# Kernel tuning notes

Measured on AMD Instinct MI355X. Metric: run time of the kernel, lower is better.

Reference implementation:

```python
import jax, jax.numpy as jnp
import numpy as np

B, L, D, H = 4, 2048, 1024, 16
DK = D // H  # 64


def setup_inputs() -> dict:
    key = jax.random.key(0)
    ks = jax.random.split(key, 8)
    s = 0.05
    return {
        "query": jax.random.normal(ks[0], (B, L, D), jnp.float32),
        "key": jax.random.normal(ks[1], (B, L, D), jnp.float32),
        "value": jax.random.normal(ks[2], (B, L, D), jnp.float32),
        "mask": jnp.ones((B, L, L), jnp.int32),
        "Wq": jax.random.normal(ks[3], (D, DK), jnp.float32) * s,
        "Wk": jax.random.normal(ks[4], (D, DK), jnp.float32) * s,
        "Wv": jax.random.normal(ks[5], (D, DK), jnp.float32) * s,
        "Wo": jax.random.normal(ks[6], (H * DK, D), jnp.float32) * s,
    }


def reference(query, key, value, mask, Wq, Wk, Wv, Wo):
    # Single-head projections (the torch module projects once, then reuses
    # the SAME q/k/v for every head, producing num_heads identical outputs).
    q = jnp.einsum("bld,dk->blk", query, Wq)   # [B, L, DK]
    k = jnp.einsum("bld,dk->blk", key, Wk)
    v = jnp.einsum("bld,dk->blk", value, Wv)
    scale = 1.0 / jnp.sqrt(jnp.asarray(DK, q.dtype))
    scores = jnp.einsum("bqk,bsk->bqs", q, k) * scale  # [B, L, L]
    scores = jnp.where(mask == 0, -jnp.inf, scores)
    p = jax.nn.softmax(scores, axis=-1)
    head = jnp.einsum("bqs,bsk->bqk", p, v)    # [B, L, DK]
    # Concatenation of H identical heads == tile along last dim.
    out = jnp.tile(head, (1, 1, H))             # [B, L, H*DK]
    return jnp.einsum("blh,hd->bld", out, Wo)
```

## Files before the change

### kernel.cpp

```cpp
#include <hip/hip_runtime.h>
#include <hip/hip_bf16.h>

#define Bb 4
#define Ll 2048
#define Dd 1024
#define DKk 64
#define BL (Bb*Ll)
#define G_SPLIT 8
#define KSPLIT 4

typedef __attribute__((ext_vector_type(4))) float f32x4;
typedef __attribute__((ext_vector_type(8))) short bf16x8;

__device__ __forceinline__ unsigned short f2bf(float x) {
  unsigned int u = __builtin_bit_cast(unsigned int, x);
  u += 0x7fffu + ((u >> 16) & 1u);
  return (unsigned short)(u >> 16);
}
__device__ __forceinline__ unsigned int pack2bf(float a, float b) {
  return (unsigned int)f2bf(a) | ((unsigned int)f2bf(b) << 16);
}

__global__ __launch_bounds__(256)
void prep_kernel(const float* __restrict__ Wq, const float* __restrict__ Wk,
                 const float* __restrict__ Wv, const float* __restrict__ Wo,
                 unsigned short* __restrict__ WqT, unsigned short* __restrict__ WkT,
                 unsigned short* __restrict__ WvT, unsigned short* __restrict__ WoSumT) {
  int idx = blockIdx.x * 256 + threadIdx.x;
  if (idx < 3 * 65536) {
    int which = idx >> 16;
    int r = idx & 65535;
    int n = r & 63, k = r >> 6;
    const float* W = which == 0 ? Wq : (which == 1 ? Wk : Wv);
    unsigned short* WT = which == 0 ? WqT : (which == 1 ? WkT : WvT);
    WT[(size_t)n * 1024 + k] = f2bf(W[(size_t)k * 64 + n]);
  } else {
    int r = idx - 3 * 65536;
    int d = r & 1023, k = r >> 10;
    float s = 0.f;
#pragma unroll
    for (int h = 0; h < 16; ++h) s += Wo[(size_t)(h * 64 + k) * 1024 + d];
    WoSumT[(size_t)d * 64 + k] = f2bf(s);
  }
}

__global__ __launch_bounds__(256)
void maskpack_kernel(const int* __restrict__ mask, unsigned long long* __restrict__ BM) {
  const int wid = (blockIdx.x * 256 + threadIdx.x) >> 6;
  const int lane = threadIdx.x & 63;
  const int nw = (gridDim.x * 256) >> 6;
  for (int task = wid; task < BL * 8; task += nw) {
    const int4 m = *(const int4*)(mask + (size_t)task * 256 + lane * 4);
    unsigned long long b0 = __ballot(m.x != 0);
    unsigned long long b1 = __ballot(m.y != 0);
    unsigned long long b2 = __ballot(m.z != 0);
    unsigned long long b3 = __ballot(m.w != 0);
    unsigned long long v = lane == 0 ? b0 : lane == 1 ? b1 : lane == 2 ? b2 : b3;
    if (lane < 4) BM[(size_t)task * 4 + lane] = v;
  }
}

__global__ __launch_bounds__(256)
void proj_kernel(const float* __restrict__ query, const float* __restrict__ key,
                 const float* __restrict__ value,
                 const unsigned short* __restrict__ WqT, const unsigned short* __restrict__ WkT,
                 const unsigned short* __restrict__ WvT,
                 float* __restrict__ Pp) {
  const int which = blockIdx.y;
  const int ks = blockIdx.z;
  const float* X = which == 0 ? query : (which == 1 ? key : value);
  const unsigned short* WT = which == 0 ? WqT : (which == 1 ? WkT : WvT);
  const int R0 = blockIdx.x * 64;

  __shared__ __align__(16) unsigned short Xl[64 * 72];
  __shared__ __align__(16) unsigned short Wl[64 * 72];

  const int tid = threadIdx.x;
  const int lane = tid & 63;
  const int w = tid >> 6;
  const int g = lane >> 4, lr = lane & 15;

  f32x4 acc[4];
#pragma unroll
  for (int t = 0; t < 4; ++t) acc[t] = (f32x4){0.f, 0.f, 0.f, 0.f};

  for (int it = 0; it < 4; ++it) {
    const int k0 = ks * 256 + it * 64;
    if (it) __syncthreads();
#pragma unroll
    for (int i = 0; i < 4; ++i) {
      int c = tid + 256 * i;
      int row = c >> 4, cc = c & 15;
      f32x4 v = *(const f32x4*)(X + (size_t)(R0 + row) * 1024 + k0 + cc * 4);
      uint2 pv;
      pv.x = pack2bf(v[0], v[1]);
      pv.y = pack2bf(v[2], v[3]);
      *(uint2*)&Xl[row * 72 + cc * 4] = pv;
    }
#pragma unroll
    for (int i = 0; i < 2; ++i) {
      int c = tid + 256 * i;
      int row = c >> 3, cc = c & 7;
      *(uint4*)&Wl[row * 72 + cc * 8] = *(const uint4*)(WT + (size_t)row * 1024 + k0 + cc * 8);
    }
    __syncthreads();
#pragma unroll
    for (int kh = 0; kh < 2; ++kh) {
      bf16x8 a = *(const bf16x8*)&Xl[(w * 16 + lr) * 72 + kh * 32 + g * 8];
#pragma unroll
      for (int t = 0; t < 4; ++t) {
        bf16x8 b = *(const bf16x8*)&Wl[(t * 16 + lr) * 72 + kh * 32 + g * 8];
        acc[t] = __builtin_amdgcn_mfma_f32_16x16x32_bf16(a, b, acc[t], 0, 0, 0);
      }
    }
  }

  float* pb = Pp + ((size_t)(which * KSPLIT + ks) * BL + R0 + w * 16) * 64;
#pragma unroll
  for (int t = 0; t < 4; ++t)
#pragma unroll
    for (int i = 0; i < 4; ++i)
      pb[(g * 4 + i) * 64 + t * 16 + lr] = acc[t][i];
}

__global__ __launch_bounds__(256)
void projcomb_kernel(const float* __restrict__ Pp,
                     unsigned short* __restrict__ Qp, unsigned short* __restrict__ Kf,
                     unsigned short* __restrict__ Vf) {
  const int which = blockIdx.y;
  int idx = blockIdx.x * 256 + threadIdx.x;
  int row = idx >> 4, c0 = (idx & 15) * 4;
  const float* base = Pp + ((size_t)which * KSPLIT * BL + row) * 64 + c0;
  f32x4 s = (f32x4){0.f, 0.f, 0.f, 0.f};
#pragma unroll
  for (int gg = 0; gg < KSPLIT; ++gg) {
    f32x4 a = *(const f32x4*)(base + (size_t)gg * BL * 64);
    s[0] += a[0]; s[1] += a[1]; s[2] += a[2]; s[3] += a[3];
  }
  const int b = row >> 11, sl = row & 2047;
  if (which == 0) {
    uint2 pv;
    pv.x = pack2bf(s[0], s[1]);
    pv.y = pack2bf(s[2], s[3]);
    *(uint2*)(Qp + (size_t)row * 64 + c0) = pv;
  } else if (which == 1) {
    const int c = (sl >> 4) & 3, lr = sl & 15, tile = b * 32 + (sl >> 6);
    const int gg = c0 >> 3, e0 = c0 & 7;
    uint2 pv;
    pv.x = pack2bf(s[0], s[1]);
    pv.y = pack2bf(s[2], s[3]);
    *(uint2*)(Kf + (size_t)tile * 4096 + (c * 8 + gg) * 128 + lr * 8 + e0) = pv;
  } else {
    const int h = (sl >> 5) & 1, g2 = (sl >> 3) & 3, e = sl & 7, tile = b * 32 + (sl >> 6);
#pragma unroll
    for (int j = 0; j < 4; ++j) {
      int dk = c0 + j, t = dk >> 4, lrv = dk & 15;
      Vf[(size_t)tile * 4096 + ((t * 2 + h) * 4 + g2) * 128 + lrv * 8 + e] = f2bf(s[j]);
    }
  }
}

__global__ __launch_bounds__(128, 4)
void attn_kernel(const unsigned short* __restrict__ Qp, const unsigned short* __restrict__ Kf,
                 const unsigned short* __restrict__ Vf, const unsigned long long* __restrict__ BM,
                 float* __restrict__ Opart, float* __restrict__ lpart) {
  const int q0 = blockIdx.x * 32;
  const int gy = blockIdx.y;
  const int b = q0 >> 11;
  const int tid = threadIdx.x, lane = tid & 63, w = tid >> 6;
  const int g = lane >> 4, lr = lane & 15;

  const unsigned short* qrow = Qp + (size_t)(q0 + w * 16 + lr) * 64;
  bf16x8 qf0 = *(const bf16x8*)(qrow + g * 8);
  bf16x8 qf1 = *(const bf16x8*)(qrow + 32 + g * 8);

  const unsigned long long* bm = BM + ((size_t)(q0 + w * 16 + lr) * 8 + gy) * 4;
  const unsigned long long W0 = bm[0], W1 = bm[1], W2 = bm[2], W3 = bm[3];

  f32x4 o[4];
#pragma unroll
  for (int t = 0; t < 4; ++t) o[t] = (f32x4){0.f, 0.f, 0.f, 0.f};
  float lsum = 0.f;

  const unsigned short* Kt = Kf + (size_t)(b * 32 + gy * 4) * 4096;
  const unsigned short* Vt = Vf + (size_t)(b * 32 + gy * 4) * 4096;

#pragma unroll
  for (int st = 0; st < 4; ++st) {
    const unsigned short* Kts = Kt + st * 4096;
    const unsigned short* Vts = Vt + st * 4096;

    bf16x8 kf0[4], kf1[4];
#pragma unroll
    for (int c = 0; c < 4; ++c) {
      kf0[c] = *(const bf16x8*)(Kts + (c * 8 + g) * 128 + lr * 8);
      kf1[c] = *(const bf16x8*)(Kts + (c * 8 + 4 + g) * 128 + lr * 8);
    }

    uint2 packs[4];
#pragma unroll
    for (int c = 0; c < 4; ++c) {
      f32x4 a4 = (f32x4){0.f, 0.f, 0.f, 0.f};
      a4 = __builtin_amdgcn_mfma_f32_16x16x32_bf16(kf0[c], qf0, a4, 0, 0, 0);
      a4 = __builtin_amdgcn_mfma_f32_16x16x32_bf16(kf1[c], qf1, a4, 0, 0, 0);
      const int j = st * 16 + 4 * c + g;
      float p0 = ((W0 >> j) & 1) ? __expf(a4[0] * 0.125f) : 0.f;
      float p1 = ((W1 >> j) & 1) ? __expf(a4[1] * 0.125f) : 0.f;
      float p2 = ((W2 >> j) & 1) ? __expf(a4[2] * 0.125f) : 0.f;
      float p3 = ((W3 >> j) & 1) ? __expf(a4[3] * 0.125f) : 0.f;
      lsum += (p0 + p1) + (p2 + p3);
      packs[c].x = pack2bf(p0, p1);
      packs[c].y = pack2bf(p2, p3);
    }

#pragma unroll
    for (int h = 0; h < 2; ++h) {
      const int srcLo = lr + ((g & 1) << 5);
      const int srcHi = srcLo + 16;
      uint2 pl0 = packs[2 * h], pl1 = packs[2 * h + 1];
      unsigned a0x = __shfl((int)pl0.x, srcLo), a0y = __shfl((int)pl0.y, srcLo);
      unsigned a1x = __shfl((int)pl1.x, srcLo), a1y = __shfl((int)pl1.y, srcLo);
      unsigned b0x = __shfl((int)pl0.x, srcHi), b0y = __shfl((int)pl0.y, srcHi);
      unsigned b1x = __shfl((int)pl1.x, srcHi), b1y = __shfl((int)pl1.y, srcHi);
      const bool hisel = ((g >> 1) & 1) != 0;
      uint4 bb;
      bb.x = hisel ? a1x : a0x;
      bb.y = hisel ? a1y : a0y;
      bb.z = hisel ? b1x : b0x;
      bb.w = hisel ? b1y : b0y;
      bf16x8 pb = __builtin_bit_cast(bf16x8, bb);
#pragma unroll
      for (int t = 0; t < 4; ++t) {
        bf16x8 av = *(const bf16x8*)(Vts + ((t * 2 + h) * 4 + g) * 128 + lr * 8);
        o[t] = __builtin_amdgcn_mfma_f32_16x16x32_bf16(av, pb, o[t], 0, 0, 0);
      }
    }
  }

  lsum += __shfl_xor(lsum, 16);
  lsum += __shfl_xor(lsum, 32);

  float* Ob = Opart + ((size_t)gy * BL + q0 + w * 16 + lr) * 64;
#pragma unroll
  for (int t = 0; t < 4; ++t)
    *(f32x4*)(Ob + t * 16 + g * 4) = o[t];
  if (lane < 16)
    lpart[(size_t)gy * BL + q0 + w * 16 + lane] = lsum;
}

__global__ __launch_bounds__(256)
void combine_kernel(const float* __restrict__ Opart, const float* __restrict__ lpart,
                    unsigned short* __restrict__ Hp) {
  int idx = blockIdx.x * 256 + threadIdx.x;
  int q = idx >> 4, c0 = (idx & 15) * 4;
  float l = 0.f;
#pragma unroll
  for (int gg = 0; gg < G_SPLIT; ++gg) l += lpart[(size_t)gg * BL + q];
  float inv = 1.f / l;
  f32x4 s = (f32x4){0.f, 0.f, 0.f, 0.f};
#pragma unroll
  for (int gg = 0; gg < G_SPLIT; ++gg) {
    f32x4 a = *(const f32x4*)(Opart + ((size_t)gg * BL + q) * 64 + c0);
    s[0] += a[0]; s[1] += a[1]; s[2] += a[2]; s[3] += a[3];
  }
  uint2 pv;
  pv.x = pack2bf(s[0] * inv, s[1] * inv);
  pv.y = pack2bf(s[2] * inv, s[3] * inv);
  *(uint2*)(Hp + (size_t)q * 64 + c0) = pv;
}

__global__ __launch_bounds__(256)
void oproj_kernel(const unsigned short* __restrict__ Hp,
                  const unsigned short* __restrict__ WoSumT, float* __restrict__ out) {
  const int R0 = blockIdx.x * 64;
  const int n0 = blockIdx.y * 256;
  __shared__ __align__(16) unsigned short Hl[64 * 72];
  __shared__ __align__(16) unsigned short Wl[256 * 72];
  const int tid = threadIdx.x, lane = tid & 63, w = tid >> 6;
  const int g = lane >> 4, lr = lane & 15;

#pragma unroll
  for (int i = 0; i < 2; ++i) {
    int c = tid + 256 * i;
    int row = c >> 3, cc = c & 7;
    *(uint4*)&Hl[row * 72 + cc * 8] = *(const uint4*)(Hp + (size_t)(R0 + row) * 64 + cc * 8);
  }
#pragma unroll
  for (int i = 0; i < 8; ++i) {
    int c = tid + 256 * i;
    int row = c >> 3, cc = c & 7;
    *(uint4*)&Wl[row * 72 + cc * 8] = *(const uint4*)(WoSumT + (size_t)(n0 + row) * 64 + cc * 8);
  }
  __syncthreads();

  f32x4 acc[16];
#pragma unroll
  for (int t = 0; t < 16; ++t) acc[t] = (f32x4){0.f, 0.f, 0.f, 0.f};
#pragma unroll
  for (int kh = 0; kh < 2; ++kh) {
    bf16x8 a = *(const bf16x8*)&Hl[(w * 16 + lr) * 72 + kh * 32 + g * 8];
#pragma unroll
    for (int t = 0; t < 16; ++t) {
      bf16x8 bb = *(const bf16x8*)&Wl[(t * 16 + lr) * 72 + kh * 32 + g * 8];
      acc[t] = __builtin_amdgcn_mfma_f32_16x16x32_bf16(a, bb, acc[t], 0, 0, 0);
    }
  }
  float* ob = out + (size_t)(R0 + w * 16 + g * 4) * 1024 + n0 + lr;
#pragma unroll
  for (int t = 0; t < 16; ++t)
#pragma unroll
    for (int i = 0; i < 4; ++i)
      ob[(size_t)i * 1024 + t * 16] = acc[t][i];
}

extern "C" void kernel_launch(void* const* d_in, const int* in_sizes, int n_in,
                              void* d_out, int out_size, void* d_ws, size_t ws_size,
                              hipStream_t stream) {
  const float* query = (const float*)d_in[0];
  const float* key   = (const float*)d_in[1];
  const float* value = (const float*)d_in[2];
  const int*   mask  = (const int*)d_in[3];
  const float* Wq    = (const float*)d_in[4];
  const float* Wk    = (const float*)d_in[5];
  const float* Wv    = (const float*)d_in[6];
  const float* Wo    = (const float*)d_in[7];
  float* out = (float*)d_out;

  unsigned short* Qp   = (unsigned short*)d_ws;
  unsigned short* Kf   = Qp + (size_t)BL * 64;
  unsigned short* Vf   = Kf + (size_t)BL * 64;
  unsigned short* WqT  = Vf + (size_t)BL * 64;
  unsigned short* WkT  = WqT + 65536;
  unsigned short* WvT  = WkT + 65536;
  unsigned short* WoSumT = WvT + 65536;
  float* lpart = (float*)(WoSumT + 65536);
  float* scratch = lpart + (size_t)G_SPLIT * BL;
  float* Pp = scratch;
  float* Opart = scratch;
  unsigned long long* BM = (unsigned long long*)(scratch + (size_t)G_SPLIT * BL * 64);
  unsigned short* Hp = Qp;

  hipLaunchKernelGGL(prep_kernel, dim3(1024), dim3(256), 0, stream,
                     Wq, Wk, Wv, Wo, WqT, WkT, WvT, WoSumT);
  hipLaunchKernelGGL(proj_kernel, dim3(128, 3, KSPLIT), dim3(256), 0, stream,
                     query, key, value, WqT, WkT, WvT, Pp);
  hipLaunchKernelGGL(projcomb_kernel, dim3(BL * 16 / 256, 3), dim3(256), 0, stream,
                     Pp, Qp, Kf, Vf);
  hipLaunchKernelGGL(maskpack_kernel, dim3(2048), dim3(256), 0, stream,
                     mask, BM);
  hipLaunchKernelGGL(attn_kernel, dim3(BL / 32, G_SPLIT), dim3(128), 0, stream,
                     Qp, Kf, Vf, BM, Opart, lpart);
  hipLaunchKernelGGL(combine_kernel, dim3(BL * 16 / 256), dim3(256), 0, stream,
                     Opart, lpart, Hp);
  hipLaunchKernelGGL(oproj_kernel, dim3(128, 4), dim3(256), 0, stream,
                     Hp, WoSumT, out);
}
```

Measured before the change: 80.71 us.

## Pre-swizzle projection weights into MFMA fragment layout and load them from global

The prep kernel now writes Wq/Wk/Wv in bf16 already arranged in the MFMA B-fragment order, so each lane fetches its 8-element operand with one contiguous 16-byte global load. This lets the projection kernel drop the weight staging through shared memory. The tile also shrinks from 64 rows with 256 threads to 32 rows with 128 threads, doubling the grid. This removes LDS traffic and a store phase, but each block now reads its weights from global memory or cache with less reuse per block.

```diff
diff --git a/kernel.cpp b/kernel.cpp
--- a/kernel.cpp
+++ b/kernel.cpp
@@ -24,16 +24,18 @@
 __global__ __launch_bounds__(256)
 void prep_kernel(const float* __restrict__ Wq, const float* __restrict__ Wk,
                  const float* __restrict__ Wv, const float* __restrict__ Wo,
-                 unsigned short* __restrict__ WqT, unsigned short* __restrict__ WkT,
-                 unsigned short* __restrict__ WvT, unsigned short* __restrict__ WoSumT) {
+                 unsigned short* __restrict__ Wfq, unsigned short* __restrict__ Wfk,
+                 unsigned short* __restrict__ Wfv, unsigned short* __restrict__ WoSumT) {
   int idx = blockIdx.x * 256 + threadIdx.x;
   if (idx < 3 * 65536) {
     int which = idx >> 16;
     int r = idx & 65535;
     int n = r & 63, k = r >> 6;
     const float* W = which == 0 ? Wq : (which == 1 ? Wk : Wv);
-    unsigned short* WT = which == 0 ? WqT : (which == 1 ? WkT : WvT);
-    WT[(size_t)n * 1024 + k] = f2bf(W[(size_t)k * 64 + n]);
+    unsigned short* Wf = which == 0 ? Wfq : (which == 1 ? Wfk : Wfv);
+    const int t = n >> 4, lr = n & 15;
+    const int kidx = k >> 5, g = (k >> 3) & 3, e = k & 7;
+    Wf[(size_t)(((kidx * 4 + t) * 4 + g) * 128) + lr * 8 + e] = f2bf(W[(size_t)k * 64 + n]);
   } else {
     int r = idx - 3 * 65536;
     int d = r & 1023, k = r >> 10;
@@ -60,20 +62,19 @@
   }
 }
 
-__global__ __launch_bounds__(256)
+__global__ __launch_bounds__(128)
 void proj_kernel(const float* __restrict__ query, const float* __restrict__ key,
                  const float* __restrict__ value,
-                 const unsigned short* __restrict__ WqT, const unsigned short* __restrict__ WkT,
-                 const unsigned short* __restrict__ WvT,
+                 const unsigned short* __restrict__ Wfq, const unsigned short* __restrict__ Wfk,
+                 const unsigned short* __restrict__ Wfv,
                  float* __restrict__ Pp) {
   const int which = blockIdx.y;
   const int ks = blockIdx.z;
   const float* X = which == 0 ? query : (which == 1 ? key : value);
-  const unsigned short* WT = which == 0 ? WqT : (which == 1 ? WkT : WvT);
-  const int R0 = blockIdx.x * 64;
-
-  __shared__ __align__(16) unsigned short Xl[64 * 72];
-  __shared__ __align__(16) unsigned short Wl[64 * 72];
+  const unsigned short* Wf = which == 0 ? Wfq : (which == 1 ? Wfk : Wfv);
+  const int R0 = blockIdx.x * 32;
+
+  __shared__ __align__(16) unsigned short Xl[32 * 72];
 
   const int tid = threadIdx.x;
   const int lane = tid & 63;
@@ -84,32 +85,28 @@
 #pragma unroll
   for (int t = 0; t < 4; ++t) acc[t] = (f32x4){0.f, 0.f, 0.f, 0.f};
 
+#pragma unroll
   for (int it = 0; it < 4; ++it) {
-    const int k0 = ks * 256 + it * 64;
+    const int K0 = ks * 256 + it * 64;
     if (it) __syncthreads();
 #pragma unroll
     for (int i = 0; i < 4; ++i) {
-      int c = tid + 256 * i;
+      int c = tid + 128 * i;
       int row = c >> 4, cc = c & 15;
-      f32x4 v = *(const f32x4*)(X + (size_t)(R0 + row) * 1024 + k0 + cc * 4);
+      f32x4 v = *(const f32x4*)(X + (size_t)(R0 + row) * 1024 + K0 + cc * 4);
       uint2 pv;
       pv.x = pack2bf(v[0], v[1]);
       pv.y = pack2bf(v[2], v[3]);
       *(uint2*)&Xl[row * 72 + cc * 4] = pv;
     }
-#pragma unroll
-    for (int i = 0; i < 2; ++i) {
-      int c = tid + 256 * i;
-      int row = c >> 3, cc = c & 7;
-      *(uint4*)&Wl[row * 72 + cc * 8] = *(const uint4*)(WT + (size_t)row * 1024 + k0 + cc * 8);
-    }
     __syncthreads();
+    const int kidx0 = K0 >> 5;
 #pragma unroll
     for (int kh = 0; kh < 2; ++kh) {
       bf16x8 a = *(const bf16x8*)&Xl[(w * 16 + lr) * 72 + kh * 32 + g * 8];
 #pragma unroll
       for (int t = 0; t < 4; ++t) {
-        bf16x8 b = *(const bf16x8*)&Wl[(t * 16 + lr) * 72 + kh * 32 + g * 8];
+        bf16x8 b = *(const bf16x8*)(Wf + (size_t)(((kidx0 + kh) * 4 + t) * 4 + g) * 128 + lr * 8);
         acc[t] = __builtin_amdgcn_mfma_f32_16x16x32_bf16(a, b, acc[t], 0, 0, 0);
       }
     }
@@ -329,10 +326,10 @@
   unsigned short* Qp   = (unsigned short*)d_ws;
   unsigned short* Kf   = Qp + (size_t)BL * 64;
   unsigned short* Vf   = Kf + (size_t)BL * 64;
-  unsigned short* WqT  = Vf + (size_t)BL * 64;
-  unsigned short* WkT  = WqT + 65536;
-  unsigned short* WvT  = WkT + 65536;
-  unsigned short* WoSumT = WvT + 65536;
+  unsigned short* Wfq  = Vf + (size_t)BL * 64;
+  unsigned short* Wfk  = Wfq + 65536;
+  unsigned short* Wfv  = Wfk + 65536;
+  unsigned short* WoSumT = Wfv + 65536;
   float* lpart = (float*)(WoSumT + 65536);
   float* scratch = lpart + (size_t)G_SPLIT * BL;
   float* Pp = scratch;
@@ -341,9 +338,9 @@
   unsigned short* Hp = Qp;
 
   hipLaunchKernelGGL(prep_kernel, dim3(1024), dim3(256), 0, stream,
-                     Wq, Wk, Wv, Wo, WqT, WkT, WvT, WoSumT);
-  hipLaunchKernelGGL(proj_kernel, dim3(128, 3, KSPLIT), dim3(256), 0, stream,
-                     query, key, value, WqT, WkT, WvT, Pp);
+                     Wq, Wk, Wv, Wo, Wfq, Wfk, Wfv, WoSumT);
+  hipLaunchKernelGGL(proj_kernel, dim3(256, 3, KSPLIT), dim3(128), 0, stream,
+                     query, key, value, Wfq, Wfk, Wfv, Pp);
   hipLaunchKernelGGL(projcomb_kernel, dim3(BL * 16 / 256, 3), dim3(256), 0, stream,
                      Pp, Qp, Kf, Vf);
   hipLaunchKernelGGL(maskpack_kernel, dim3(2048), dim3(256), 0, stream,
```

Measured after the change: 82.74 us. 2.5% more time.
